# Performance work log

Measured on AMD Instinct MI355X. Metric: run time of the kernel, lower is better.

The kernel has to match this reference:

```python
import jax, jax.numpy as jnp
import numpy as np

N, I, D, K = 64, 8192, 128, 16


def setup_inputs() -> dict:
    key = jax.random.key(0)
    k1, k2 = jax.random.split(key)
    x = jax.random.normal(k1, (N, I, D), dtype=jnp.float32)
    # each point belongs to one of k clusters of its own batch element -> offset n*K
    ci = jax.random.randint(k2, (N, I), 0, K) + jnp.arange(N)[:, None] * K
    return {
        "feature_matrix_batch": x,
        "cluster_index": ci.reshape(-1).astype(jnp.int32),  # [N*I]
        "k": K,
    }


def reference(feature_matrix_batch, cluster_index, k):
    n, i, d = feature_matrix_batch.shape
    flat = feature_matrix_batch.reshape(-1, d)  # [N*I, D]
    # scatter_max over segment ids -> [N*k, D]
    out = jax.ops.segment_max(flat, cluster_index, num_segments=n * k)
    return out.reshape(n, k, d)
```

## Files before the change

### kernel.cpp

```cpp
#include <hip/hip_runtime.h>
#include <stdint.h>

#define NB 64
#define NI 8192
#define ND 128
#define NK 16
#define PTS_PER_BLOCK 256
#define BLOCKS_PER_BATCH (NI / PTS_PER_BLOCK)
#define OUT_ELEMS (NB * NK * ND)
#define MAPPED_NEG_INF 0x007FFFFFu

__device__ __forceinline__ uint32_t map_f32(float f) {
    uint32_t b = __float_as_uint(f);
    return b ^ ((uint32_t)((int32_t)b >> 31) | 0x80000000u);
}

__global__ __launch_bounds__(256) void seg_init(uint32_t* __restrict__ out) {
    int idx = blockIdx.x * 256 + threadIdx.x;
    out[idx] = MAPPED_NEG_INF;
}

__global__ __launch_bounds__(256, 8) void seg_max_kernel(
        const float* __restrict__ x,
        const int* __restrict__ ci,
        uint32_t* __restrict__ out) {
    __shared__ uint32_t loc[NK * ND];
    __shared__ int cidx[PTS_PER_BLOCK];

    const int t = threadIdx.x;
    const int b = blockIdx.x;
    const int batch = b >> 5;
    const int chunk = (b & (BLOCKS_PER_BATCH - 1)) * PTS_PER_BLOCK;
    const int row0 = batch * NI + chunk;

    for (int i = t; i < NK * ND; i += 256) loc[i] = MAPPED_NEG_INF;
    cidx[t] = ci[row0 + t] - batch * NK;
    __syncthreads();

    const int lane32 = t & 31;
    const int rsub = t >> 5;

    const float4* xrow = (const float4*)(x + (size_t)row0 * ND) + lane32;

    for (int it = 0; it < PTS_PER_BLOCK / 8; ++it) {
        const int i = it * 8 + rsub;
        const int c = cidx[i];
        float4 v = xrow[(size_t)i * (ND / 4)];
        uint32_t m0 = map_f32(v.x);
        uint32_t m1 = map_f32(v.y);
        uint32_t m2 = map_f32(v.z);
        uint32_t m3 = map_f32(v.w);
        if ((unsigned)c < (unsigned)NK) {
            uint32_t* lp = &loc[(c << 7) + lane32];
            atomicMax(&lp[0],  m0);
            atomicMax(&lp[32], m1);
            atomicMax(&lp[64], m2);
            atomicMax(&lp[96], m3);
        }
    }
    __syncthreads();

    uint32_t* ob = out + (size_t)batch * (NK * ND);
    for (int o = t; o < NK * ND; o += 256) {
        const int c = o >> 7;
        const int d = o & 127;
        const int li = (c << 7) + ((d & 3) << 5) + (d >> 2);
        uint32_t v = loc[li];
        if (v != MAPPED_NEG_INF) atomicMax(&ob[o], v);
    }
}

__global__ __launch_bounds__(256) void seg_decode(uint32_t* __restrict__ out) {
    int idx = blockIdx.x * 256 + threadIdx.x;
    uint32_t m = out[idx];
    uint32_t b = (m & 0x80000000u) ? (m ^ 0x80000000u) : ~m;
    out[idx] = b;
}

extern "C" void kernel_launch(void* const* d_in, const int* in_sizes, int n_in,
                              void* d_out, int out_size, void* d_ws, size_t ws_size,
                              hipStream_t stream) {
    const float* x = (const float*)d_in[0];
    const int* ci = (const int*)d_in[1];
    uint32_t* out = (uint32_t*)d_out;

    seg_init<<<OUT_ELEMS / 256, 256, 0, stream>>>(out);
    seg_max_kernel<<<NB * BLOCKS_PER_BATCH, 256, 0, stream>>>(x, ci, out);
    seg_decode<<<OUT_ELEMS / 256, 256, 0, stream>>>(out);
}
```

Baseline: 55.71 us.

## Replace global atomic merge with workspace partials and a separate reduce kernel

```diff
diff --git a/kernel.cpp b/kernel.cpp
--- a/kernel.cpp
+++ b/kernel.cpp
@@ -5,14 +5,79 @@
 #define NI 8192
 #define ND 128
 #define NK 16
-#define PTS_PER_BLOCK 256
-#define BLOCKS_PER_BATCH (NI / PTS_PER_BLOCK)
-#define OUT_ELEMS (NB * NK * ND)
+#define SEG (NK * ND)
+#define OUT_ELEMS (NB * SEG)
 #define MAPPED_NEG_INF 0x007FFFFFu
+
+#define PPB_A 512
+#define BPB_A (NI / PPB_A)
+#define GRID_A (NB * BPB_A)
+#define WS_NEEDED ((size_t)GRID_A * SEG * 4)
+
+#define PPB_B 256
+#define BPB_B (NI / PPB_B)
 
 __device__ __forceinline__ uint32_t map_f32(float f) {
     uint32_t b = __float_as_uint(f);
     return b ^ ((uint32_t)((int32_t)b >> 31) | 0x80000000u);
+}
+__device__ __forceinline__ uint32_t unmap_u32(uint32_t m) {
+    return (m & 0x80000000u) ? (m ^ 0x80000000u) : ~m;
+}
+
+__global__ __launch_bounds__(256, 4) void seg_partial(
+        const float* __restrict__ x,
+        const int* __restrict__ ci,
+        uint32_t* __restrict__ ws) {
+    __shared__ uint32_t loc[SEG];
+    __shared__ int cidx[PPB_A];
+
+    const int t = threadIdx.x;
+    const int b = blockIdx.x;
+    const int batch = b >> 4;
+    const int chunk = (b & (BPB_A - 1)) * PPB_A;
+    const int row0 = batch * NI + chunk;
+
+    for (int i = t; i < SEG; i += 256) loc[i] = MAPPED_NEG_INF;
+    for (int i = t; i < PPB_A; i += 256) cidx[i] = ci[row0 + i] - batch * NK;
+    __syncthreads();
+
+    const int lane32 = t & 31;
+    const int rsub = t >> 5;
+    const float4* xrow = (const float4*)(x + (size_t)row0 * ND) + lane32;
+
+    #pragma unroll 2
+    for (int it = 0; it < PPB_A / 8; ++it) {
+        const int i = it * 8 + rsub;
+        const int c = cidx[i];
+        float4 v = xrow[(size_t)i * (ND / 4)];
+        uint32_t* lp = &loc[(c << 7) + lane32];
+        atomicMax(&lp[0],  map_f32(v.x));
+        atomicMax(&lp[32], map_f32(v.y));
+        atomicMax(&lp[64], map_f32(v.z));
+        atomicMax(&lp[96], map_f32(v.w));
+    }
+    __syncthreads();
+
+    uint32_t* wb = ws + (size_t)b * SEG;
+    for (int o = t; o < SEG; o += 256) {
+        const int c = o >> 7;
+        const int d = o & 127;
+        wb[o] = loc[(c << 7) + ((d & 3) << 5) + (d >> 2)];
+    }
+}
+
+__global__ __launch_bounds__(256) void seg_reduce(
+        const uint32_t* __restrict__ ws,
+        uint32_t* __restrict__ out) {
+    const int idx = blockIdx.x * 256 + threadIdx.x;
+    const int batch = idx >> 11;
+    const int o = idx & (SEG - 1);
+    const uint32_t* p = ws + (size_t)batch * BPB_A * SEG + o;
+    uint32_t m = MAPPED_NEG_INF;
+    #pragma unroll
+    for (int j = 0; j < BPB_A; ++j) m = max(m, p[(size_t)j * SEG]);
+    out[idx] = unmap_u32(m);
 }
 
 __global__ __launch_bounds__(256) void seg_init(uint32_t* __restrict__ out) {
@@ -24,57 +89,47 @@
         const float* __restrict__ x,
         const int* __restrict__ ci,
         uint32_t* __restrict__ out) {
-    __shared__ uint32_t loc[NK * ND];
-    __shared__ int cidx[PTS_PER_BLOCK];
+    __shared__ uint32_t loc[SEG];
+    __shared__ int cidx[PPB_B];
 
     const int t = threadIdx.x;
     const int b = blockIdx.x;
     const int batch = b >> 5;
-    const int chunk = (b & (BLOCKS_PER_BATCH - 1)) * PTS_PER_BLOCK;
+    const int chunk = (b & (BPB_B - 1)) * PPB_B;
     const int row0 = batch * NI + chunk;
 
-    for (int i = t; i < NK * ND; i += 256) loc[i] = MAPPED_NEG_INF;
+    for (int i = t; i < SEG; i += 256) loc[i] = MAPPED_NEG_INF;
     cidx[t] = ci[row0 + t] - batch * NK;
     __syncthreads();
 
     const int lane32 = t & 31;
     const int rsub = t >> 5;
-
     const float4* xrow = (const float4*)(x + (size_t)row0 * ND) + lane32;
 
-    for (int it = 0; it < PTS_PER_BLOCK / 8; ++it) {
+    for (int it = 0; it < PPB_B / 8; ++it) {
         const int i = it * 8 + rsub;
         const int c = cidx[i];
         float4 v = xrow[(size_t)i * (ND / 4)];
-        uint32_t m0 = map_f32(v.x);
-        uint32_t m1 = map_f32(v.y);
-        uint32_t m2 = map_f32(v.z);
-        uint32_t m3 = map_f32(v.w);
-        if ((unsigned)c < (unsigned)NK) {
-            uint32_t* lp = &loc[(c << 7) + lane32];
-            atomicMax(&lp[0],  m0);
-            atomicMax(&lp[32], m1);
-            atomicMax(&lp[64], m2);
-            atomicMax(&lp[96], m3);
-        }
+        uint32_t* lp = &loc[(c << 7) + lane32];
+        atomicMax(&lp[0],  map_f32(v.x));
+        atomicMax(&lp[32], map_f32(v.y));
+        atomicMax(&lp[64], map_f32(v.z));
+        atomicMax(&lp[96], map_f32(v.w));
     }
     __syncthreads();
 
-    uint32_t* ob = out + (size_t)batch * (NK * ND);
-    for (int o = t; o < NK * ND; o += 256) {
+    uint32_t* ob = out + (size_t)batch * SEG;
+    for (int o = t; o < SEG; o += 256) {
         const int c = o >> 7;
         const int d = o & 127;
-        const int li = (c << 7) + ((d & 3) << 5) + (d >> 2);
-        uint32_t v = loc[li];
+        uint32_t v = loc[(c << 7) + ((d & 3) << 5) + (d >> 2)];
         if (v != MAPPED_NEG_INF) atomicMax(&ob[o], v);
     }
 }
 
 __global__ __launch_bounds__(256) void seg_decode(uint32_t* __restrict__ out) {
     int idx = blockIdx.x * 256 + threadIdx.x;
-    uint32_t m = out[idx];
-    uint32_t b = (m & 0x80000000u) ? (m ^ 0x80000000u) : ~m;
-    out[idx] = b;
+    out[idx] = unmap_u32(out[idx]);
 }
 
 extern "C" void kernel_launch(void* const* d_in, const int* in_sizes, int n_in,
@@ -84,7 +139,13 @@
     const int* ci = (const int*)d_in[1];
     uint32_t* out = (uint32_t*)d_out;
 
-    seg_init<<<OUT_ELEMS / 256, 256, 0, stream>>>(out);
-    seg_max_kernel<<<NB * BLOCKS_PER_BATCH, 256, 0, stream>>>(x, ci, out);
-    seg_decode<<<OUT_ELEMS / 256, 256, 0, stream>>>(out);
+    if (ws_size >= WS_NEEDED) {
+        uint32_t* ws = (uint32_t*)d_ws;
+        seg_partial<<<GRID_A, 256, 0, stream>>>(x, ci, ws);
+        seg_reduce<<<OUT_ELEMS / 256, 256, 0, stream>>>(ws, out);
+    } else {
+        seg_init<<<OUT_ELEMS / 256, 256, 0, stream>>>(out);
+        seg_max_kernel<<<NB * BPB_B, 256, 0, stream>>>(x, ci, out);
+        seg_decode<<<OUT_ELEMS / 256, 256, 0, stream>>>(out);
+    }
 }
```

Result: faster. 52.95 us (-5.0%).
